# Kernel tuning notes

Hardware: AMD Instinct MI355X
Metric: run time of the kernel (lower is better)

The kernel has to match this reference:

```python
import jax, jax.numpy as jnp
import numpy as np

N_SEG = 128      # number of ragged segments (len(leng))
TOTAL = 32768    # total rows = sum(leng)
D = 1280         # cnn_feature (tf_efficientnet_b0 classifier.in_features)
D_HEAD = 512     # hidden of logits head


def setup_inputs() -> dict:
    key = jax.random.key(0)
    ks = jax.random.split(key, 8)
    # ragged lengths (static at trace time), summing exactly to TOTAL
    rng = np.random.default_rng(0)
    leng = rng.integers(64, 448, size=N_SEG).astype(np.int64)
    leng = np.maximum((leng * (TOTAL / leng.sum())).astype(np.int64), 1)
    leng[-1] += TOTAL - leng.sum()
    segment_ids = jnp.asarray(np.repeat(np.arange(N_SEG), leng), jnp.int32)

    features = jax.random.normal(ks[0], (TOTAL, D), jnp.float32)
    s = 0.02
    Ww = jax.random.normal(ks[1], (D, D), jnp.float32) * s        # proj_w.weight
    bw = jnp.zeros((D,), jnp.float32)                              # proj_w.bias
    v = jax.random.normal(ks[2], (D,), jnp.float32) * s           # proj_v.weight (1,D) squeezed
    W1 = jax.random.normal(ks[3], (D_HEAD, D), jnp.float32) * s   # logits[0].weight
    b1 = jnp.zeros((D_HEAD,), jnp.float32)
    W2 = jax.random.normal(ks[4], (1, D_HEAD), jnp.float32) * s   # logits[3].weight
    b2 = jnp.zeros((1,), jnp.float32)
    return {"features": features, "Ww": Ww, "bw": bw, "v": v,
            "W1": W1, "b1": b1, "W2": W2, "b2": b2,
            "segment_ids": segment_ids}


def reference(features, Ww, bw, v, W1, b1, W2, b2, segment_ids):
    # per-row attention logits: tanh(x @ Ww^T + bw) @ v    -> [TOTAL]
    H = jnp.tanh(features @ Ww.T + bw)
    s = H @ v
    # segment-wise stable softmax (replaces Python loop over leng)
    m = jax.ops.segment_max(s, segment_ids, num_segments=N_SEG)
    e = jnp.exp(s - m[segment_ids])
    z = jax.ops.segment_sum(e, segment_ids, num_segments=N_SEG)
    att = e / z[segment_ids]                                      # [TOTAL]
    # attention-weighted sum pooling per segment -> [N_SEG, D]
    pooled = jax.ops.segment_sum(features * att[:, None], segment_ids,
                                 num_segments=N_SEG)
    # logits head (dropout is identity in eval)
    h = jax.nn.relu(pooled @ W1.T + b1)
    return h @ W2.T + b2                                          # [N_SEG, 1]
```

## Files before the change

kernel.cpp:

```cpp
#include <hip/hip_runtime.h>
#include <hip/hip_bf16.h>


#define TOTAL_ROWS 32768
#define DIM 1280
#define NSEG 128
#define DHEAD 512
#define NKT 20
#define NPART 4

typedef _Float16 f16x8 __attribute__((ext_vector_type(8)));
typedef _Float16 f16x4 __attribute__((ext_vector_type(4)));
typedef float f32x4 __attribute__((ext_vector_type(4)));

#define OFF_XH   0
#define OFF_WH   83886080
#define OFF_S    87162880
#define OFF_SEG  87425024
#define OFF_POOL 87426048
#define OFF_H    88081408
#define OFF_PP   OFF_WH

__device__ __forceinline__ void load_lds16(const void* g, void* l) {
  __builtin_amdgcn_global_load_lds(
      (const __attribute__((address_space(1))) unsigned int*)g,
      (__attribute__((address_space(3))) unsigned int*)l, 16, 0, 0);
}

__device__ __forceinline__ float tanh_fast(float x) {
  float e = __expf(2.0f * x);
  return 1.0f - 2.0f * __builtin_amdgcn_rcpf(e + 1.0f);
}

__global__ void cvt_init_kernel(const float* __restrict__ a, _Float16* __restrict__ oa,
                                int na8, const float* __restrict__ b,
                                _Float16* __restrict__ ob, int nb8,
                                const int* __restrict__ sid,
                                int* __restrict__ segstart, float* __restrict__ s) {
  int i = blockIdx.x * blockDim.x + threadIdx.x;
  if (i < TOTAL_ROWS) {
    s[i] = 0.f;
    int sg = sid[i];
    if (i == 0) segstart[0] = 0;
    else if (sid[i - 1] != sg) segstart[sg] = i;
    if (i == TOTAL_ROWS - 1) segstart[sg + 1] = TOTAL_ROWS;
  }
  const float* in;
  _Float16* out;
  int idx;
  if (i < na8) {
    in = a; out = oa; idx = i;
  } else {
    idx = i - na8;
    if (idx >= nb8) return;
    in = b; out = ob;
  }
  const float4* p = (const float4*)in + (size_t)idx * 2;
  float4 u0 = p[0], u1 = p[1];
  f16x8 h;
  h[0] = (_Float16)u0.x; h[1] = (_Float16)u0.y;
  h[2] = (_Float16)u0.z; h[3] = (_Float16)u0.w;
  h[4] = (_Float16)u1.x; h[5] = (_Float16)u1.y;
  h[6] = (_Float16)u1.z; h[7] = (_Float16)u1.w;
  *((f16x8*)out + idx) = h;
}

__global__ __launch_bounds__(512, 2) void gemm_s_kernel(
    const _Float16* __restrict__ X, const _Float16* __restrict__ W,
    const float* __restrict__ v, const float* __restrict__ bw,
    float* __restrict__ s) {
  __shared__ _Float16 As[2][2][8192];
  __shared__ _Float16 Bs[2][2][8192];

  const int rowBase = blockIdx.x * 256;
  const int jBase = blockIdx.y * 256;
  const int t = threadIdx.x;
  const int lane = t & 63;
  const int w = t >> 6;
  const int wm = w >> 2;
  const int wn = w & 3;
  const int lm = lane & 15;
  const int kc = lane >> 4;
  const int bh = wn >> 1;

  const int subrow = lane >> 3;
  const int g = ((lane & 7) - subrow) & 7;
  const _Float16* gA = X + (size_t)(rowBase + w * 8 + subrow) * DIM + g * 8;
  const _Float16* gB = W + (size_t)(jBase + w * 8 + subrow) * DIM + g * 8;

  int aOff[2], bOff[2];
#pragma unroll
  for (int ks = 0; ks < 2; ++ks) {
    int swz = ((ks * 4 + kc + lm) & 7) * 8;
    aOff[ks] = lm * 64 + swz;
    bOff[ks] = ((wn & 1) * 64 + lm) * 64 + swz;
  }

  f32x4 acc[8][4];
  const f32x4 zero = {0.f, 0.f, 0.f, 0.f};
#pragma unroll
  for (int i = 0; i < 8; ++i)
#pragma unroll
    for (int j = 0; j < 4; ++j) acc[i][j] = zero;

  f16x8 a[4][2], b[4][2];

#define STAGE_A(BUF, HALF, TT) do { \
    const _Float16* _src = gA + (size_t)(HALF) * 128 * DIM + (size_t)(TT) * 64; \
    load_lds16(_src, &As[BUF][HALF][w * 512]); \
    load_lds16(_src + 64 * DIM, &As[BUF][HALF][4096 + w * 512]); \
  } while (0)
#define STAGE_B(BUF, HALF, TT) do { \
    const _Float16* _src = gB + (size_t)(HALF) * 128 * DIM + (size_t)(TT) * 64; \
    load_lds16(_src, &Bs[BUF][HALF][w * 512]); \
    load_lds16(_src + 64 * DIM, &Bs[BUF][HALF][4096 + w * 512]); \
  } while (0)

#define PH_READ_A(BUF, MTB) do { \
    _Pragma("unroll") for (int mt = 0; mt < 4; ++mt) \
    _Pragma("unroll") for (int ks = 0; ks < 2; ++ks) \
      a[mt][ks] = *(const f16x8*)&As[BUF][wm][aOff[ks] + (MTB + mt) * 1024]; \
  } while (0)
#define PH_READ_B(BUF, NTB) do { \
    _Pragma("unroll") for (int nt = 0; nt < 2; ++nt) \
    _Pragma("unroll") for (int ks = 0; ks < 2; ++ks) \
      b[NTB + nt][ks] = *(const f16x8*)&Bs[BUF][bh][bOff[ks] + (NTB + nt) * 1024]; \
  } while (0)
#define PH_MFMA(MTB, NTB) do { \
    __builtin_amdgcn_s_setprio(1); \
    _Pragma("unroll") for (int mt = 0; mt < 4; ++mt) \
    _Pragma("unroll") for (int nt = 0; nt < 2; ++nt) \
    _Pragma("unroll") for (int ks = 0; ks < 2; ++ks) \
      acc[MTB + mt][NTB + nt] = __builtin_amdgcn_mfma_f32_16x16x32_f16( \
          a[mt][ks], b[NTB + nt][ks], acc[MTB + mt][NTB + nt], 0, 0, 0); \
    __builtin_amdgcn_s_setprio(0); \
  } while (0)

#define CFENCE asm volatile("" ::: "memory")
#define LGKM0  asm volatile("s_waitcnt lgkmcnt(0)" ::: "memory")
#define WAIT_VM4 asm volatile("s_waitcnt vmcnt(4)" ::: "memory")
#define WAIT_VM0 asm volatile("s_waitcnt vmcnt(0)" ::: "memory")
#define BAR __builtin_amdgcn_s_barrier()

#define KTILE(BUF, S0, S1, S3, TAILWAIT) do { \
    CFENCE; \
     \
    PH_READ_A(BUF, 0); PH_READ_B(BUF, 0); S0; \
    BAR; LGKM0; PH_MFMA(0, 0); BAR; \
     \
    PH_READ_B(BUF, 2); S1; \
    BAR; LGKM0; PH_MFMA(0, 2); BAR; \
     \
    PH_READ_A(BUF, 4); \
    BAR; LGKM0; PH_MFMA(4, 0); BAR; \
     \
    S3; \
    BAR; LGKM0; PH_MFMA(4, 2); \
    TAILWAIT; BAR; \
  } while (0)

  STAGE_A(0, 0, 0); STAGE_A(0, 1, 0);
  STAGE_B(0, 0, 0); STAGE_B(0, 1, 0);
  STAGE_A(1, 0, 1); STAGE_A(1, 1, 1);
  WAIT_VM4;
  BAR;

  for (int kt = 0; kt < NKT - 2; kt += 2) {
    KTILE(0,
          STAGE_B(1, 0, kt + 1),
          STAGE_B(1, 1, kt + 1),
          { STAGE_A(0, 0, kt + 2); STAGE_A(0, 1, kt + 2); },
          WAIT_VM4);
    KTILE(1,
          STAGE_B(0, 0, kt + 2),
          STAGE_B(0, 1, kt + 2),
          { STAGE_A(1, 0, kt + 3); STAGE_A(1, 1, kt + 3); },
          WAIT_VM4);
  }
  KTILE(0, STAGE_B(1, 0, NKT - 1), STAGE_B(1, 1, NKT - 1), (void)0, WAIT_VM0);
  KTILE(1, (void)0, (void)0, (void)0, (void)0);

#undef KTILE
#undef STAGE_A
#undef STAGE_B
#undef PH_READ_A
#undef PH_READ_B
#undef PH_MFMA

  const int colBase = jBase + wn * 64 + lm;
  float vv[4], bb[4];
#pragma unroll
  for (int nt = 0; nt < 4; ++nt) {
    int j = colBase + nt * 16;
    vv[nt] = v[j];
    bb[nt] = bw[j];
  }
  const int gq = lane >> 4;
#pragma unroll
  for (int mt = 0; mt < 8; ++mt) {
#pragma unroll
    for (int r = 0; r < 4; ++r) {
      float sumv = 0.f;
#pragma unroll
      for (int nt = 0; nt < 4; ++nt)
        sumv += tanh_fast(acc[mt][nt][r] + bb[nt]) * vv[nt];
      sumv += __shfl_xor(sumv, 1);
      sumv += __shfl_xor(sumv, 2);
      sumv += __shfl_xor(sumv, 4);
      sumv += __shfl_xor(sumv, 8);
      if (lm == 0) {
        int row = rowBase + wm * 128 + mt * 16 + gq * 4 + r;
        atomicAdd(&s[row], sumv);
      }
    }
  }
}

__global__ void softpool_kernel(const _Float16* __restrict__ F,
                                const float* __restrict__ s,
                                const int* __restrict__ segstart,
                                float* __restrict__ pooledp) {
  int seg = blockIdx.x, part = blockIdx.y;
  int st = segstart[seg], en = segstart[seg + 1];
  int t = threadIdx.x;
  __shared__ float redm[5], redz[5];
  float m = -1e30f;
  for (int i = st + t; i < en; i += 320) m = fmaxf(m, s[i]);
  for (int d = 1; d < 64; d <<= 1) m = fmaxf(m, __shfl_xor(m, d));
  if ((t & 63) == 0) redm[t >> 6] = m;
  __syncthreads();
  m = fmaxf(fmaxf(fmaxf(redm[0], redm[1]), fmaxf(redm[2], redm[3])), redm[4]);
  float z = 0.f;
  for (int i = st + t; i < en; i += 320) z += __expf(s[i] - m);
  for (int d = 1; d < 64; d <<= 1) z += __shfl_xor(z, d);
  if ((t & 63) == 0) redz[t >> 6] = z;
  __syncthreads();
  z = redz[0] + redz[1] + redz[2] + redz[3] + redz[4];
  float rz = 1.0f / z;

  int len = en - st;
  int chunk = (len + NPART - 1) / NPART;
  int r0 = st + chunk * part;
  int r1 = min(en, r0 + chunk);
  float acc[4] = {0.f, 0.f, 0.f, 0.f};
  int r = r0;
  for (; r + 2 <= r1; r += 2) {
    float a0 = __expf(s[r] - m) * rz;
    float a1 = __expf(s[r + 1] - m) * rz;
    f16x4 f0 = ((const f16x4*)(F + (size_t)r * DIM))[t];
    f16x4 f1 = ((const f16x4*)(F + (size_t)(r + 1) * DIM))[t];
#pragma unroll
    for (int c = 0; c < 4; ++c) {
      acc[c] = fmaf(a0, (float)f0[c], acc[c]);
      acc[c] = fmaf(a1, (float)f1[c], acc[c]);
    }
  }
  if (r < r1) {
    float a0 = __expf(s[r] - m) * rz;
    f16x4 f0 = ((const f16x4*)(F + (size_t)r * DIM))[t];
#pragma unroll
    for (int c = 0; c < 4; ++c) acc[c] = fmaf(a0, (float)f0[c], acc[c]);
  }
  float4 o;
  o.x = acc[0]; o.y = acc[1]; o.z = acc[2]; o.w = acc[3];
  *(float4*)(pooledp + ((size_t)part * NSEG + seg) * DIM + t * 4) = o;
}

__global__ void fold_kernel(const float* __restrict__ pp,
                            float* __restrict__ pooled) {
  int i = blockIdx.x * 256 + threadIdx.x;
  pooled[i] = pp[i] + pp[i + NSEG * DIM] + pp[i + 2 * NSEG * DIM] +
              pp[i + 3 * NSEG * DIM];
}

__global__ void head1_kernel(const float* __restrict__ pooled,
                             const float* __restrict__ W1,
                             const float* __restrict__ b1, float* __restrict__ h) {
  int og = blockIdx.x, sg = blockIdx.y;
  __shared__ float Wt[16 * 65];
  __shared__ float Pt[32 * 65];
  int t = threadIdx.x;
  int tx = t & 15, ty = t >> 4;
  float acc0 = 0.f, acc1 = 0.f;
  for (int kcc = 0; kcc < 20; ++kcc) {
    __syncthreads();
#pragma unroll
    for (int u = 0; u < 4; ++u) {
      int lin = t + 256 * u;
      int o = lin >> 6, kk = lin & 63;
      Wt[o * 65 + kk] = W1[(size_t)(og * 16 + o) * DIM + kcc * 64 + kk];
    }
#pragma unroll
    for (int u = 0; u < 8; ++u) {
      int lin = t + 256 * u;
      int ss = lin >> 6, kk = lin & 63;
      Pt[ss * 65 + kk] = pooled[(size_t)(sg * 32 + ss) * DIM + kcc * 64 + kk];
    }
    __syncthreads();
#pragma unroll
    for (int kk = 0; kk < 64; ++kk) {
      float wv = Wt[tx * 65 + kk];
      acc0 = fmaf(Pt[ty * 65 + kk], wv, acc0);
      acc1 = fmaf(Pt[(ty + 16) * 65 + kk], wv, acc1);
    }
  }
  int o = og * 16 + tx;
  float bias = b1[o];
  h[(size_t)(sg * 32 + ty) * DHEAD + o] = fmaxf(acc0 + bias, 0.f);
  h[(size_t)(sg * 32 + ty + 16) * DHEAD + o] = fmaxf(acc1 + bias, 0.f);
}

__global__ void head2_kernel(const float* __restrict__ h,
                             const float* __restrict__ W2,
                             const float* __restrict__ b2, float* __restrict__ out) {
  int seg = blockIdx.x;
  int t = threadIdx.x;
  float val = h[(size_t)seg * DHEAD + t] * W2[t] +
              h[(size_t)seg * DHEAD + t + 256] * W2[t + 256];
  for (int d = 1; d < 64; d <<= 1) val += __shfl_xor(val, d);
  __shared__ float red[4];
  if ((t & 63) == 0) red[t >> 6] = val;
  __syncthreads();
  if (t == 0) out[seg] = red[0] + red[1] + red[2] + red[3] + b2[0];
}

extern "C" void kernel_launch(void* const* d_in, const int* in_sizes, int n_in,
                              void* d_out, int out_size, void* d_ws, size_t ws_size,
                              hipStream_t stream) {
  const float* features = (const float*)d_in[0];
  const float* Ww = (const float*)d_in[1];
  const float* bw = (const float*)d_in[2];
  const float* v = (const float*)d_in[3];
  const float* W1 = (const float*)d_in[4];
  const float* b1 = (const float*)d_in[5];
  const float* W2 = (const float*)d_in[6];
  const float* b2 = (const float*)d_in[7];
  const int* segids = (const int*)d_in[8];
  float* out = (float*)d_out;

  char* ws = (char*)d_ws;
  _Float16* Xh = (_Float16*)(ws + OFF_XH);
  _Float16* Wh = (_Float16*)(ws + OFF_WH);
  float* s = (float*)(ws + OFF_S);
  int* segstart = (int*)(ws + OFF_SEG);
  float* pooled = (float*)(ws + OFF_POOL);
  float* pooledp = (float*)(ws + OFF_PP);
  float* h = (float*)(ws + OFF_H);

  const int na8 = TOTAL_ROWS * DIM / 8;
  const int nb8 = DIM * DIM / 8;
  cvt_init_kernel<<<(na8 + nb8 + 255) / 256, 256, 0, stream>>>(
      features, Xh, na8, Ww, Wh, nb8, segids, segstart, s);

  dim3 ggrid(TOTAL_ROWS / 256, DIM / 256);
  gemm_s_kernel<<<ggrid, 512, 0, stream>>>(Xh, Wh, v, bw, s);

  softpool_kernel<<<dim3(NSEG, NPART), 320, 0, stream>>>(Xh, s, segstart, pooledp);
  fold_kernel<<<NSEG * DIM / 256, 256, 0, stream>>>(pooledp, pooled);
  head1_kernel<<<dim3(32, 4), 256, 0, stream>>>(pooled, W1, b1, h);
  head2_kernel<<<NSEG, 256, 0, stream>>>(h, W2, b2, out);
}
```

Measured before the change: 473.8 us.

## Collapse GEMM k-tile into two phases and prefetch B one tile ahead

Each k-tile of the projection GEMM now loads all four B fragments at once and runs two MFMA phases instead of four, with two barriers per tile instead of eight. The global-to-LDS staging order changes so that B for the next-next tile and A for the next tile are issued during the current tile. This is meant to cut barrier and synchronisation overhead and give the MFMAs longer uninterrupted runs. In exchange, more B registers stay live at once, and the finer interleaving of LDS reads with MFMA work across waves is lost.

New measurement: 463.1 us. 1.02x faster.

```diff
diff --git a/kernel.cpp b/kernel.cpp
--- a/kernel.cpp
+++ b/kernel.cpp
@@ -121,18 +121,18 @@
     _Pragma("unroll") for (int ks = 0; ks < 2; ++ks) \
       a[mt][ks] = *(const f16x8*)&As[BUF][wm][aOff[ks] + (MTB + mt) * 1024]; \
   } while (0)
-#define PH_READ_B(BUF, NTB) do { \
-    _Pragma("unroll") for (int nt = 0; nt < 2; ++nt) \
+#define PH_READ_B(BUF) do { \
+    _Pragma("unroll") for (int nt = 0; nt < 4; ++nt) \
     _Pragma("unroll") for (int ks = 0; ks < 2; ++ks) \
-      b[NTB + nt][ks] = *(const f16x8*)&Bs[BUF][bh][bOff[ks] + (NTB + nt) * 1024]; \
-  } while (0)
-#define PH_MFMA(MTB, NTB) do { \
+      b[nt][ks] = *(const f16x8*)&Bs[BUF][bh][bOff[ks] + nt * 1024]; \
+  } while (0)
+#define PH_MFMA(MTB) do { \
     __builtin_amdgcn_s_setprio(1); \
     _Pragma("unroll") for (int mt = 0; mt < 4; ++mt) \
-    _Pragma("unroll") for (int nt = 0; nt < 2; ++nt) \
+    _Pragma("unroll") for (int nt = 0; nt < 4; ++nt) \
     _Pragma("unroll") for (int ks = 0; ks < 2; ++ks) \
-      acc[MTB + mt][NTB + nt] = __builtin_amdgcn_mfma_f32_16x16x32_f16( \
-          a[mt][ks], b[NTB + nt][ks], acc[MTB + mt][NTB + nt], 0, 0, 0); \
+      acc[MTB + mt][nt] = __builtin_amdgcn_mfma_f32_16x16x32_f16( \
+          a[mt][ks], b[nt][ks], acc[MTB + mt][nt], 0, 0, 0); \
     __builtin_amdgcn_s_setprio(0); \
   } while (0)
 
@@ -142,43 +142,38 @@
 #define WAIT_VM0 asm volatile("s_waitcnt vmcnt(0)" ::: "memory")
 #define BAR __builtin_amdgcn_s_barrier()
 
-#define KTILE(BUF, S0, S1, S3, TAILWAIT) do { \
+#define KTILE(BUF, SA, SB, TAILWAIT) do { \
     CFENCE; \
      \
-    PH_READ_A(BUF, 0); PH_READ_B(BUF, 0); S0; \
-    BAR; LGKM0; PH_MFMA(0, 0); BAR; \
+    PH_READ_A(BUF, 0); PH_READ_B(BUF); SA; \
+    LGKM0; PH_MFMA(0); \
+    BAR; \
      \
-    PH_READ_B(BUF, 2); S1; \
-    BAR; LGKM0; PH_MFMA(0, 2); BAR; \
-     \
-    PH_READ_A(BUF, 4); \
-    BAR; LGKM0; PH_MFMA(4, 0); BAR; \
-     \
-    S3; \
-    BAR; LGKM0; PH_MFMA(4, 2); \
+    PH_READ_A(BUF, 4); SB; \
+    LGKM0; PH_MFMA(4); \
     TAILWAIT; BAR; \
   } while (0)
 
   STAGE_A(0, 0, 0); STAGE_A(0, 1, 0);
   STAGE_B(0, 0, 0); STAGE_B(0, 1, 0);
-  STAGE_A(1, 0, 1); STAGE_A(1, 1, 1);
+  STAGE_B(1, 0, 1); STAGE_B(1, 1, 1);
   WAIT_VM4;
   BAR;
 
   for (int kt = 0; kt < NKT - 2; kt += 2) {
     KTILE(0,
-          STAGE_B(1, 0, kt + 1),
-          STAGE_B(1, 1, kt + 1),
-          { STAGE_A(0, 0, kt + 2); STAGE_A(0, 1, kt + 2); },
+          { STAGE_A(1, 0, kt + 1); STAGE_A(1, 1, kt + 1); },
+          { STAGE_B(0, 0, kt + 2); STAGE_B(0, 1, kt + 2); },
           WAIT_VM4);
     KTILE(1,
-          STAGE_B(0, 0, kt + 2),
-          STAGE_B(0, 1, kt + 2),
-          { STAGE_A(1, 0, kt + 3); STAGE_A(1, 1, kt + 3); },
+          { STAGE_A(0, 0, kt + 2); STAGE_A(0, 1, kt + 2); },
+          { STAGE_B(1, 0, kt + 3); STAGE_B(1, 1, kt + 3); },
           WAIT_VM4);
   }
-  KTILE(0, STAGE_B(1, 0, NKT - 1), STAGE_B(1, 1, NKT - 1), (void)0, WAIT_VM0);
-  KTILE(1, (void)0, (void)0, (void)0, (void)0);
+  KTILE(0,
+        { STAGE_A(1, 0, NKT - 1); STAGE_A(1, 1, NKT - 1); },
+        (void)0, WAIT_VM0);
+  KTILE(1, (void)0, (void)0, (void)0);
 
 #undef KTILE
 #undef STAGE_A
```
